# Optimization experiments

Hardware: AMD Instinct MI355X
Metric: run time of the kernel (lower is better)

## Reference

```python
import jax, jax.numpy as jnp
import numpy as np
from jax import lax

MAX_C = 16       # MAX_MERGE_NUMS
COND_THRES = 0.2
IOU_THRES = 0.3
CLASS_OFFSET = 1e4  # shift per-class so cross-class BEV IoU == 0 (emulates per-class loop)


def setup_inputs() -> dict:
    key = jax.random.key(0)
    k1, k2, k3, k4, k5 = jax.random.split(key, 5)
    B, N = 4, 4096
    # realistic 3D boxes: centers, positive sizes, heading
    centers = jax.random.normal(k1, (B, N, 3), jnp.float32) * 20.0
    sizes = jax.random.uniform(k2, (B, N, 3), jnp.float32, 0.5, 4.5)
    heading = jax.random.uniform(k3, (B, N, 1), jnp.float32, -np.pi, np.pi)
    boxes = jnp.concatenate([centers, sizes, heading], -1)  # [B,N,7]
    scores = jax.random.uniform(k4, (B, N), jnp.float32)
    labels = jax.random.randint(k5, (B, N), 0, 3, jnp.int32)
    kw = jax.random.split(jax.random.fold_in(key, 1), 2)
    W1 = jax.random.normal(kw[0], (7, 64), jnp.float32) * 0.3
    b1 = jnp.zeros((64,), jnp.float32)
    W2 = jax.random.normal(kw[1], (64, 1), jnp.float32) * 0.3
    b2 = jnp.zeros((1,), jnp.float32)
    return {"boxes": boxes, "scores": scores, "labels": labels,
            "W1": W1, "b1": b1, "W2": W2, "b2": b2}


def _nms_merge_frame(boxes, scores, labels, W1, b1, W2, b2):
    # boxes [N,7], scores [N], labels [N] int32
    N = boxes.shape[0]
    valid = scores > COND_THRES                       # cond_mask
    skey = jnp.where(valid, scores, -jnp.inf)
    order = jnp.argsort(-skey)                        # score descending
    boxes, scores = boxes[order], scores[order]
    labels, valid = labels[order], valid[order]

    # nearest-BEV (axis-aligned) IoU; class offset keeps classes disjoint
    off = labels.astype(boxes.dtype) * CLASS_OFFSET
    cx, cy = boxes[:, 0] + off, boxes[:, 1]
    hx, hy = boxes[:, 3] * 0.5, boxes[:, 4] * 0.5
    x1, x2, y1, y2 = cx - hx, cx + hx, cy - hy, cy + hy
    ix = jnp.clip(jnp.minimum(x2[:, None], x2[None]) - jnp.maximum(x1[:, None], x1[None]), 0.0)
    iy = jnp.clip(jnp.minimum(y2[:, None], y2[None]) - jnp.maximum(y1[:, None], y1[None]), 0.0)
    inter = ix * iy                                   # [N,N]
    area = (x2 - x1) * (y2 - y1)
    iou = inter / jnp.clip(area[:, None] + area[None] - inter, 1e-6)
    overlap = iou > IOU_THRES                         # includes self

    # greedy clustering: highest-score remaining box leads its cluster
    def body(i, st):
        alive, cid = st
        lead = alive[i]
        take = alive & overlap[i] & lead
        cid = jnp.where(take, i, cid)
        return alive & (~take), cid
    alive, cid = lax.fori_loop(0, N, body,
                               (valid, jnp.full((N,), -1, jnp.int32)))
    leader = cid == jnp.arange(N, dtype=jnp.int32)    # cluster representatives

    # rank of each box within its cluster (score order preserved)
    idx = jnp.arange(N)
    same = (cid[None, :] == cid[:, None]) & (cid[:, None] >= 0)
    rank = (same & (idx[None, :] < idx[:, None])).sum(-1)  # [N]

    # scatter up to MAX_C members per cluster (zero-padded buffers)
    dest = jnp.where((cid >= 0) & (rank < MAX_C), cid, N)  # N = dump row
    clusters = jnp.zeros((N + 1, MAX_C, 7), boxes.dtype)
    clusters = clusters.at[dest, jnp.minimum(rank, MAX_C - 1)].set(boxes)[:N]

    # merge network: per-box MLP -> softmax weights over cluster slots
    h = jax.nn.relu(clusters @ W1 + b1)               # [N,MAX_C,64]
    logits = (h @ W2 + b2)[..., 0]                    # [N,MAX_C]
    slot_ok = jnp.any(clusters != 0, -1)
    logits = jnp.where(slot_ok, logits, -1e9)
    w = jax.nn.softmax(logits, -1)
    merged = jnp.einsum('nc,ncd->nd', w, clusters)    # [N,7]

    # masked scatter: non-positive merged sizes fall back to leader sizes
    size = jnp.where(merged[:, 3:6] <= 0, boxes[:, 3:6], merged[:, 3:6])
    out_box = jnp.concatenate([merged[:, :3], size, merged[:, 6:7]], -1)
    info = jnp.concatenate([out_box, scores[:, None],
                            labels.astype(boxes.dtype)[:, None]], -1)  # [N,9]
    info = jnp.where(leader[:, None], info, 0.0)
    return info, leader


def reference(boxes, scores, labels, W1, b1, W2, b2):
    info, leader = jax.vmap(_nms_merge_frame,
                            in_axes=(0, 0, 0, None, None, None, None))(
        boxes, scores, labels, W1, b1, W2, b2)
    return info, leader
```

## Files before the change

kernel.cpp:

```cpp
#include <hip/hip_runtime.h>
#include <stdint.h>

#pragma clang fp contract(off)

#define BF 4
#define NN 4096
#define MAXC 16
#define PL 2048
#define WL 32
#define WF 24
#define TRI_CAP (64 * (WL * (WL + 1) / 2))

typedef unsigned long long u64;
typedef uint32_t u32;

#define WAVE_SYNC() asm volatile("s_waitcnt lgkmcnt(0)" ::: "memory")

__device__ __forceinline__ u64 shfl64(u64 v, int src) {
  return (u64)__shfl((long long)v, src, 64);
}
__device__ __forceinline__ u64 readlane64(u64 v, int l) {
  u32 lo = (u32)__builtin_amdgcn_readlane((int)(u32)v, l);
  u32 hi = (u32)__builtin_amdgcn_readlane((int)(u32)(v >> 32), l);
  return ((u64)hi << 32) | lo;
}
__device__ __forceinline__ u64 greedy64_iso(u64 D, u64 rem, u64 onlyme) {
  u64 lead = 0;
  while (rem) {
    u64 t = D & rem;
    u64 iso = __ballot(t == onlyme) & rem;
    lead |= iso;
    rem &= ~iso;
    if (!rem) break;
    int b = __builtin_ctzll(rem);
    lead |= 1ull << b;
    rem &= ~readlane64(D, b);
    if (!rem) break;
    b = __builtin_ctzll(rem);
    lead |= 1ull << b;
    rem &= ~readlane64(D, b);
  }
  return lead;
}

__global__ __launch_bounds__(256) void rank_kernel(
    const float* __restrict__ scores, u64* __restrict__ keyS)
{
  __shared__ u64 keys[NN];
  __shared__ int cnt[4][64];
  const int f = blockIdx.x >> 6, rb = blockIdx.x & 63;
  const int tid = threadIdx.x, wave = tid >> 6, lane = tid & 63;
  for (int s = 0; s < 16; s++) {
    int idx = tid + 256 * s;
    float sc = scores[f * NN + idx];
    bool valid = sc > 0.2f;
    u32 bits = __float_as_uint(sc);
    u32 m = bits ^ ((bits >> 31) ? 0xFFFFFFFFu : 0x80000000u);
    u32 hi = valid ? ~m : 0xFFFFFFFFu;
    keys[idx] = ((u64)hi << 32) | (u32)idx;
  }
  __syncthreads();
  const int row = rb * 64 + lane;
  const u64 mykey = keys[row];
  int c = 0;
  const int j0 = wave * 1024;
#pragma unroll 8
  for (int j = j0; j < j0 + 1024; j++)
    c += (keys[j] < mykey) ? 1 : 0;
  cnt[wave][lane] = c;
  __syncthreads();
  if (wave == 0) {
    int rank = cnt[0][lane] + cnt[1][lane] + cnt[2][lane] + cnt[3][lane];
    keyS[f * NN + rank] = mykey;
  }
}

__global__ __launch_bounds__(256) void countscan_kernel(
    const u64* __restrict__ keyS, const int* __restrict__ labels,
    int* __restrict__ chunkOffG, int* __restrict__ VbufL)
{
  __shared__ int cnt[64][3];
  const int f = blockIdx.x, tid = threadIdx.x;
  const int wave = tid >> 6, lane = tid & 63;
  for (int s = 0; s < 16; s++) {
    int chunk = wave * 16 + s;
    int p = chunk * 64 + lane;
    u64 kv = keyS[f * NN + p];
    bool valid = (u32)(kv >> 32) != 0xFFFFFFFFu;
    int g = (int)(kv & 0xFFFFFFFFull);
    int l = valid ? labels[f * NN + g] : 3;
    u64 B0 = __ballot((l & 1) != 0);
    u64 B1 = __ballot((l & 2) != 0);
    if (lane < 3) {
      u64 Mb = ((lane & 1) ? B0 : ~B0) & ((lane & 2) ? B1 : ~B1);
      cnt[chunk][lane] = __popcll(Mb);
    }
  }
  __syncthreads();
  if (wave == 0) {
    for (int ll = 0; ll < 3; ll++) {
      int v = cnt[lane][ll];
      int incl = v;
      for (int off2 = 1; off2 < 64; off2 <<= 1) {
        int up = __shfl_up(incl, off2, 64);
        if (lane >= off2) incl += up;
      }
      chunkOffG[(f * 64 + lane) * 3 + ll] = incl - v;
      if (lane == 63) VbufL[f * 3 + ll] = incl;
    }
  }
}

__global__ __launch_bounds__(256) void gather_kernel(
    const u64* __restrict__ keyS, const float* __restrict__ boxes,
    const float* __restrict__ scores, const int* __restrict__ labels,
    const int* __restrict__ chunkOffG,
    float* __restrict__ sboxes, float* __restrict__ sscore, float* __restrict__ slabel,
    int* __restrict__ lab_slot, int* __restrict__ loc_slot,
    int* __restrict__ pglob,
    float* __restrict__ px1, float* __restrict__ px2, float* __restrict__ py1,
    float* __restrict__ py2, float* __restrict__ parea)
{
  const int gs = blockIdx.x * 256 + threadIdx.x;
  const int f = gs >> 12, p = gs & (NN - 1);
  const int lane = threadIdx.x & 63, chunk = p >> 6;
  const u64 ltmask = (1ull << lane) - 1ull;
  u64 kv = keyS[gs];
  bool valid = (u32)(kv >> 32) != 0xFFFFFFFFu;
  int g = (int)(kv & 0xFFFFFFFFull);
  const float* bp = boxes + (size_t)(f * NN + g) * 7;
  float b0 = bp[0], b1v = bp[1], b2v = bp[2], b3 = bp[3], b4 = bp[4], b5 = bp[5], b6 = bp[6];
  int lab = labels[f * NN + g];
  const int o = f * NN + p;
  float* sb = sboxes + (size_t)o * 7;
  sb[0] = b0; sb[1] = b1v; sb[2] = b2v; sb[3] = b3; sb[4] = b4; sb[5] = b5; sb[6] = b6;
  sscore[o] = scores[f * NN + g];
  slabel[o] = (float)lab;
  int l = valid ? lab : 3;
  u64 B0 = __ballot((l & 1) != 0);
  u64 B1 = __ballot((l & 2) != 0);
  u64 M = ((l & 1) ? B0 : ~B0) & ((l & 2) ? B1 : ~B1);
  int rank = __popcll(M & ltmask);
  if (l < 3) {
    int loc = chunkOffG[(f * 64 + chunk) * 3 + l] + rank;
    int pi = (f * 3 + l) * PL + loc;
    float off = (float)l * 10000.0f;
    float cx = b0 + off, cy = b1v;
    float hx = b3 * 0.5f, hy = b4 * 0.5f;
    float x1 = cx - hx, x2 = cx + hx, y1 = cy - hy, y2 = cy + hy;
    float area = (x2 - x1) * (y2 - y1);
    pglob[pi] = p;
    px1[pi] = x1; px2[pi] = x2; py1[pi] = y1; py2[pi] = y2; parea[pi] = area;
    lab_slot[o] = l; loc_slot[o] = loc;
  } else {
    lab_slot[o] = -1; loc_slot[o] = -1;
  }
}

__global__ __launch_bounds__(256) void mask_kernel(
    const float* __restrict__ px1, const float* __restrict__ px2,
    const float* __restrict__ py1, const float* __restrict__ py2,
    const float* __restrict__ parea, const int* __restrict__ pglob,
    const int* __restrict__ VbufL,
    u64* __restrict__ maskP, u64* __restrict__ triT)
{
  __shared__ float4 cbox[1024];
  __shared__ float carea[1024];
  const int bx = blockIdx.x;
  const int fl = bx >> 8, rem = bx & 255;
  const int rt = rem >> 1, wt = rem & 1;
  const int r0 = rt * 16;
  const int Vl = VbufL[fl];
  if (r0 >= Vl) return;
  if (wt * 1024 >= Vl) return;
  const int tid = threadIdx.x;
  for (int q = tid; q < 1024; q += 256) {
    int c = fl * PL + wt * 1024 + q;
    cbox[q] = make_float4(px1[c], px2[c], py1[c], py2[c]);
    carea[q] = parea[c];
  }
  __syncthreads();
  const int row = r0 + (tid & 15);
  const int wl = tid >> 4;
  const int cw = wt * 16 + wl;
  const int nc = Vl - cw * 64;
  if (row >= Vl || nc <= 0) return;
  const int rg = fl * PL + row;
  const float rx1 = px1[rg], rx2 = px2[rg], ry1 = py1[rg], ry2 = py2[rg], ra = parea[rg];
  u64 bits = 0;
  const int qb = wl * 64;
  for (int b = 0; b < 64; b++) {
    float4 cb = cbox[qb + b];
    float ca = carea[qb + b];
    float ix = fminf(rx2, cb.y) - fmaxf(rx1, cb.x);
    ix = fmaxf(ix, 0.0f);
    float iy = fminf(ry2, cb.w) - fmaxf(ry1, cb.z);
    iy = fmaxf(iy, 0.0f);
    float inter = ix * iy;
    float den = fmaxf((ra + ca) - inter, 1e-6f);
    float iou = inter / den;
    bits |= ((u64)(iou > 0.3f)) << b;
  }
  if (nc < 64) bits &= (1ull << nc) - 1ull;
  const int f = fl / 3;
  const int p = pglob[fl * PL + row];
  maskP[((size_t)f * NN + p) * WL + cw] = bits;
  if (row >= 64 * cw) {
    const int W = (Vl + 63) >> 6;
    int base = 64 * (cw * W - (cw * (cw - 1)) / 2);
    triT[(size_t)fl * TRI_CAP + base + (row - 64 * cw)] = bits;
  }
}

__global__ __launch_bounds__(64) void nms_kernel(
    const u64* __restrict__ triT, const int* __restrict__ VbufL,
    u64* __restrict__ leadersP)
{
  __shared__ u64 tri[64 * (WF * (WF + 1) / 2) + 128];
  const int fl = blockIdx.x, lane = threadIdx.x;
  const int Vl = VbufL[fl];
  const int W = (Vl + 63) >> 6;
  const u64* mT = triT + (size_t)fl * TRI_CAP;
  const u64 onlyme = 1ull << lane;
  u64 alive = 0;
  if (lane < WL) {
    int rb = Vl - 64 * lane;
    alive = (rb >= 64) ? ~0ull : ((rb > 0) ? ((1ull << rb) - 1ull) : 0ull);
  }
  u64 myLead = 0;

  if (W > 0 && W <= WF) {
    const int totw = 64 * (W * (W + 1) / 2);
    const int nch = (totw * 8 + 1023) >> 10;
    const char* g = (const char*)mT;
    char* l = (char*)tri;
    int batch = 0;
    for (int it = 0; it < nch; it++) {
      __builtin_amdgcn_global_load_lds(
          (const __attribute__((address_space(1))) unsigned int*)(g + (size_t)it * 1024 + (size_t)lane * 16),
          (__attribute__((address_space(3))) unsigned int*)(l + (size_t)it * 1024),
          16, 0, 0);
      if (++batch == 48) {
        asm volatile("s_waitcnt vmcnt(0)" ::: "memory");
        batch = 0;
      }
    }
    asm volatile("s_waitcnt vmcnt(0)" ::: "memory");
    int offw = 0;
    u64 D = tri[lane];
    for (int w = 0; w < W; w++) {
      const int offw_next = offw + 64 * (W - w);
      u64 Dnext = (w + 1 < W) ? tri[offw_next + lane] : 0;
      u64 lead = greedy64_iso(D, readlane64(alive, w), onlyme);
      if (lane == w) myLead = lead;
      if (lead) {
        const u64* strm = tri + offw;
        int v = w + 1;
        for (; v + 3 < W; v += 4) {
          u64 a0 = strm[64 * (v - w) + lane];
          u64 a1 = strm[64 * (v + 1 - w) + lane];
          u64 a2 = strm[64 * (v + 2 - w) + lane];
          u64 a3 = strm[64 * (v + 3 - w) + lane];
          u64 c0 = __ballot((a0 & lead) != 0ull);
          u64 c1 = __ballot((a1 & lead) != 0ull);
          u64 c2 = __ballot((a2 & lead) != 0ull);
          u64 c3 = __ballot((a3 & lead) != 0ull);
          if (lane == v)     alive &= ~c0;
          if (lane == v + 1) alive &= ~c1;
          if (lane == v + 2) alive &= ~c2;
          if (lane == v + 3) alive &= ~c3;
        }
        for (; v < W; v++) {
          u64 a0 = strm[64 * (v - w) + lane];
          u64 c0 = __ballot((a0 & lead) != 0ull);
          if (lane == v) alive &= ~c0;
        }
      }
      D = Dnext;
      offw = offw_next;
    }
  } else if (W > 0) {
    int offw = 0;
    for (int w = 0; w < W; w++) {
      const u64* strm = mT + offw;
      u64 D = strm[lane];
      u64 lead = greedy64_iso(D, readlane64(alive, w), onlyme);
      if (lane == w) myLead = lead;
      if (lead) {
        for (int v = w + 1; v < W; v++) {
          u64 a0 = strm[64 * (v - w) + lane];
          u64 c0 = __ballot((a0 & lead) != 0ull);
          if (lane == v) alive &= ~c0;
        }
      }
      offw += 64 * (W - w);
    }
  }
  if (lane < WL) leadersP[fl * WL + lane] = myLead;
}

__global__ __launch_bounds__(256) void cid_kernel(
    const u64* __restrict__ maskP, const u64* __restrict__ leadersP,
    const int* __restrict__ lab_slot, const int* __restrict__ loc_slot,
    const int* __restrict__ VbufL, int* __restrict__ cidP)
{
  const int g = blockIdx.x * 4 + (threadIdx.x >> 6);
  const int lane = threadIdx.x & 63;
  const int f = g >> 12, p = g & (NN - 1);
  const int l = lab_slot[f * NN + p];
  if (l < 0) return;
  const int fl = f * 3 + l;
  const int loc = loc_slot[f * NN + p];
  const int Wl = (VbufL[fl] + 63) >> 6;
  u64 L = 0, m = 0;
  if (lane < Wl) {
    L = leadersP[fl * WL + lane];
    m = maskP[((size_t)f * NN + p) * WL + lane];
  }
  const int g6 = loc >> 6, b6 = loc & 63;
  u64 pmask = (lane < g6) ? ~0ull
            : (lane == g6 ? ((b6 == 63) ? ~0ull : ((1ull << (b6 + 1)) - 1ull)) : 0ull);
  u64 v = m & L & pmask;
  u64 bl = __ballot(v != 0ull);
  int cid = -1;
  if (bl != 0ull) {
    int w = __builtin_ctzll(bl);
    u64 vw = shfl64(v, w);
    cid = w * 64 + __builtin_ctzll(vw);
  }
  if (lane == 0) cidP[fl * PL + loc] = cid;
}

__global__ __launch_bounds__(256) void mm_kernel(
    const u64* __restrict__ maskP, const u64* __restrict__ leadersP,
    const int* __restrict__ cidP, const int* __restrict__ lab_slot,
    const int* __restrict__ loc_slot, const int* __restrict__ pglob,
    const int* __restrict__ VbufL,
    const float* __restrict__ sboxes, const float* __restrict__ sscore,
    const float* __restrict__ slabel,
    const float* __restrict__ W1, const float* __restrict__ b1,
    const float* __restrict__ W2, const float* __restrict__ b2,
    float* __restrict__ out)
{
  __shared__ int   mlistS[4][MAXC];
  __shared__ float mbS[4][MAXC][7];
  __shared__ float lgS[4][MAXC];
  __shared__ float wnS[4][MAXC];
  const int wv = threadIdx.x >> 6, lane = threadIdx.x & 63;
  const int bi = blockIdx.x * 4 + wv;
  const int f = bi >> 12, i = bi & (NN - 1);
  const int o = f * NN + i;
  float* info = out + (size_t)o * 9;
  float* lead = out + (size_t)BF * NN * 9 + o;
  const int l = lab_slot[o];
  bool isLead = false;
  int loc = 0, fl = 0;
  if (l >= 0) {
    fl = f * 3 + l;
    loc = loc_slot[o];
    isLead = (leadersP[fl * WL + (loc >> 6)] >> (loc & 63)) & 1ull;
  }
  if (!isLead) {
    if (lane < 9) info[lane] = 0.0f;
    if (lane == 0) *lead = 0.0f;
    return;
  }
  int* mlist = mlistS[wv];
  float (*mb)[7] = mbS[wv];
  float* lg = lgS[wv];
  float* wn = wnS[wv];
  const u64* mrow = maskP + (size_t)o * WL;
  const int Wl = (VbufL[fl] + 63) >> 6;
  int total = 0;
  for (int w = loc >> 6; w < Wl && total < MAXC; w++) {
    u64 word = mrow[w];
    int pos = w * 64 + lane;
    bool cand = ((word >> lane) & 1ull) && (cidP[fl * PL + pos] == loc);
    u64 mbal = __ballot(cand);
    int r = __popcll(mbal & ((1ull << lane) - 1ull));
    int slot = total + r;
    if (cand && slot < MAXC) mlist[slot] = pglob[fl * PL + pos];
    total += __popcll(mbal);
  }
  const int cnt = min(total, MAXC);
  WAVE_SYNC();
  if (lane < cnt) {
    int j = mlist[lane];
    const float* bp = sboxes + (size_t)(f * NN + j) * 7;
    for (int d = 0; d < 7; d++) mb[lane][d] = bp[d];
  }
  float w1r[7];
  for (int d = 0; d < 7; d++) w1r[d] = W1[d * 64 + lane];
  const float b1c = b1[lane], w2c = W2[lane], b2v = b2[0];
  WAVE_SYNC();
  for (int s = 0; s < cnt; s++) {
    float t = b1c;
    for (int d = 0; d < 7; d++) t += mb[s][d] * w1r[d];
    float h = fmaxf(t, 0.0f);
    float v = h * w2c;
    for (int off2 = 32; off2 > 0; off2 >>= 1) v += __shfl_xor(v, off2, 64);
    if (lane == 0) lg[s] = v + b2v;
  }
  WAVE_SYNC();
  float mx = -1e30f;
  for (int s = 0; s < cnt; s++) mx = fmaxf(mx, lg[s]);
  float den = 0.0f;
  for (int s = 0; s < cnt; s++) den += expf(lg[s] - mx);
  if (lane < cnt) wn[lane] = expf(lg[lane] - mx) / den;
  WAVE_SYNC();
  float val = 0.0f;
  if (lane < 7) {
    float acc = 0.0f;
    for (int s = 0; s < cnt; s++) acc += wn[s] * mb[s][lane];
    val = acc;
    if (lane >= 3 && lane <= 5 && val <= 0.0f) val = sboxes[(size_t)o * 7 + lane];
  } else if (lane == 7) {
    val = sscore[o];
  } else if (lane == 8) {
    val = slabel[o];
  }
  if (lane < 9) info[lane] = val;
  if (lane == 0) *lead = 1.0f;
}

extern "C" void kernel_launch(void* const* d_in, const int* in_sizes, int n_in,
                              void* d_out, int out_size, void* d_ws, size_t ws_size,
                              hipStream_t stream)
{
  const float* boxes  = (const float*)d_in[0];
  const float* scores = (const float*)d_in[1];
  const int*   labels = (const int*)d_in[2];
  const float* W1     = (const float*)d_in[3];
  const float* b1     = (const float*)d_in[4];
  const float* W2     = (const float*)d_in[5];
  const float* b2     = (const float*)d_in[6];
  float* out = (float*)d_out;

  char* ws = (char*)d_ws;
  size_t off = 0;
  auto alloc = [&](size_t bytes) -> void* {
    void* p = ws + off;
    off = (off + bytes + 255) & ~(size_t)255;
    return p;
  };
  u64*   keyS    = (u64*)  alloc((size_t)BF * NN * 8);
  int*   chunkOffG=(int*)  alloc((size_t)BF * 64 * 3 * 4);
  float* sboxes  = (float*)alloc((size_t)BF * NN * 7 * 4);
  float* sscore  = (float*)alloc((size_t)BF * NN * 4);
  float* slabel  = (float*)alloc((size_t)BF * NN * 4);
  int*   lab_slot= (int*)  alloc((size_t)BF * NN * 4);
  int*   loc_slot= (int*)  alloc((size_t)BF * NN * 4);
  int*   pglob   = (int*)  alloc((size_t)BF * 3 * PL * 4);
  float* px1     = (float*)alloc((size_t)BF * 3 * PL * 4);
  float* px2     = (float*)alloc((size_t)BF * 3 * PL * 4);
  float* py1     = (float*)alloc((size_t)BF * 3 * PL * 4);
  float* py2     = (float*)alloc((size_t)BF * 3 * PL * 4);
  float* parea   = (float*)alloc((size_t)BF * 3 * PL * 4);
  int*   VbufL   = (int*)  alloc((size_t)BF * 3 * 4);
  u64*   leadersP= (u64*)  alloc((size_t)BF * 3 * WL * 8);
  int*   cidP    = (int*)  alloc((size_t)BF * 3 * PL * 4);
  u64*   maskP   = (u64*)  alloc((size_t)BF * NN * WL * 8);
  u64*   triT    = (u64*)  alloc((size_t)BF * 3 * TRI_CAP * 8);
  (void)  alloc(32768);

  rank_kernel<<<BF * 64, 256, 0, stream>>>(scores, keyS);
  countscan_kernel<<<BF, 256, 0, stream>>>(keyS, labels, chunkOffG, VbufL);
  gather_kernel<<<BF * NN / 256, 256, 0, stream>>>(keyS, boxes, scores, labels,
                                                   chunkOffG, sboxes, sscore,
                                                   slabel, lab_slot, loc_slot,
                                                   pglob, px1, px2, py1, py2,
                                                   parea);
  mask_kernel<<<BF * 3 * 256, 256, 0, stream>>>(px1, px2, py1, py2, parea,
                                                pglob, VbufL, maskP, triT);
  nms_kernel<<<BF * 3, 64, 0, stream>>>(triT, VbufL, leadersP);
  cid_kernel<<<BF * NN / 4, 256, 0, stream>>>(maskP, leadersP, lab_slot,
                                              loc_slot, VbufL, cidP);
  mm_kernel<<<BF * NN / 4, 256, 0, stream>>>(maskP, leadersP, cidP, lab_slot,
                                             loc_slot, pglob, VbufL, sboxes,
                                             sscore, slabel, W1, b1, W2, b2, out);
}
```

Baseline: 159.6 us.

## Fuse rank, per-label count/scan and gather into one kernel

Label bits are packed into the low bits of each sort key. The rank kernel now counts, for each element, both its global rank and its rank within its own label, and scatters the boxes and per-class arrays directly. This removes the countscan and gather kernels, the keyS and chunkOffG intermediates, and two launches. Each thread does slightly more work in the O(N) comparison loop. Separately, the mask kernel now loads only the valid columns into shared memory.

After: 156.8 us. Within noise of the previous version (-1.8%).

```diff
diff --git a/kernel.cpp b/kernel.cpp
--- a/kernel.cpp
+++ b/kernel.cpp
@@ -43,117 +43,91 @@
   return lead;
 }
 
-__global__ __launch_bounds__(256) void rank_kernel(
-    const float* __restrict__ scores, u64* __restrict__ keyS)
+__global__ __launch_bounds__(256) void rg_kernel(
+    const float* __restrict__ scores, const float* __restrict__ boxes,
+    const int* __restrict__ labels,
+    float* __restrict__ sboxes, float* __restrict__ sscore, float* __restrict__ slabel,
+    int* __restrict__ lab_slot, int* __restrict__ loc_slot,
+    int* __restrict__ pglob,
+    float* __restrict__ px1, float* __restrict__ px2, float* __restrict__ py1,
+    float* __restrict__ py2, float* __restrict__ parea,
+    int* __restrict__ VbufL)
 {
   __shared__ u64 keys[NN];
   __shared__ int cnt[4][64];
+  __shared__ int lcnt[4][64];
+  __shared__ int vc[4][3];
   const int f = blockIdx.x >> 6, rb = blockIdx.x & 63;
   const int tid = threadIdx.x, wave = tid >> 6, lane = tid & 63;
   for (int s = 0; s < 16; s++) {
     int idx = tid + 256 * s;
     float sc = scores[f * NN + idx];
     bool valid = sc > 0.2f;
+    int lab = labels[f * NN + idx];
     u32 bits = __float_as_uint(sc);
     u32 m = bits ^ ((bits >> 31) ? 0xFFFFFFFFu : 0x80000000u);
     u32 hi = valid ? ~m : 0xFFFFFFFFu;
-    keys[idx] = ((u64)hi << 32) | (u32)idx;
+    u32 lo = ((u32)idx << 2) | (valid ? (u32)lab : 3u);
+    keys[idx] = ((u64)hi << 32) | lo;
   }
   __syncthreads();
+  if (rb == 0) {
+    int c0 = 0, c1 = 0, c2 = 0;
+    const int base = wave * 1024;
+    for (int s = 0; s < 16; s++) {
+      u32 lb = (u32)keys[base + s * 64 + lane] & 3u;
+      c0 += (lb == 0); c1 += (lb == 1); c2 += (lb == 2);
+    }
+    for (int off = 32; off; off >>= 1) {
+      c0 += __shfl_xor(c0, off, 64);
+      c1 += __shfl_xor(c1, off, 64);
+      c2 += __shfl_xor(c2, off, 64);
+    }
+    if (lane == 0) { vc[wave][0] = c0; vc[wave][1] = c1; vc[wave][2] = c2; }
+  }
   const int row = rb * 64 + lane;
   const u64 mykey = keys[row];
-  int c = 0;
+  const u32 mylab = (u32)mykey & 3u;
+  int c = 0, lc = 0;
   const int j0 = wave * 1024;
 #pragma unroll 8
-  for (int j = j0; j < j0 + 1024; j++)
-    c += (keys[j] < mykey) ? 1 : 0;
+  for (int j = j0; j < j0 + 1024; j++) {
+    u64 kj = keys[j];
+    bool lt = kj < mykey;
+    c += lt ? 1 : 0;
+    lc += (lt && (((u32)kj & 3u) == mylab)) ? 1 : 0;
+  }
   cnt[wave][lane] = c;
+  lcnt[wave][lane] = lc;
   __syncthreads();
+  if (rb == 0 && wave == 1 && lane < 3)
+    VbufL[f * 3 + lane] = vc[0][lane] + vc[1][lane] + vc[2][lane] + vc[3][lane];
   if (wave == 0) {
     int rank = cnt[0][lane] + cnt[1][lane] + cnt[2][lane] + cnt[3][lane];
-    keyS[f * NN + rank] = mykey;
-  }
-}
-
-__global__ __launch_bounds__(256) void countscan_kernel(
-    const u64* __restrict__ keyS, const int* __restrict__ labels,
-    int* __restrict__ chunkOffG, int* __restrict__ VbufL)
-{
-  __shared__ int cnt[64][3];
-  const int f = blockIdx.x, tid = threadIdx.x;
-  const int wave = tid >> 6, lane = tid & 63;
-  for (int s = 0; s < 16; s++) {
-    int chunk = wave * 16 + s;
-    int p = chunk * 64 + lane;
-    u64 kv = keyS[f * NN + p];
-    bool valid = (u32)(kv >> 32) != 0xFFFFFFFFu;
-    int g = (int)(kv & 0xFFFFFFFFull);
-    int l = valid ? labels[f * NN + g] : 3;
-    u64 B0 = __ballot((l & 1) != 0);
-    u64 B1 = __ballot((l & 2) != 0);
-    if (lane < 3) {
-      u64 Mb = ((lane & 1) ? B0 : ~B0) & ((lane & 2) ? B1 : ~B1);
-      cnt[chunk][lane] = __popcll(Mb);
-    }
-  }
-  __syncthreads();
-  if (wave == 0) {
-    for (int ll = 0; ll < 3; ll++) {
-      int v = cnt[lane][ll];
-      int incl = v;
-      for (int off2 = 1; off2 < 64; off2 <<= 1) {
-        int up = __shfl_up(incl, off2, 64);
-        if (lane >= off2) incl += up;
-      }
-      chunkOffG[(f * 64 + lane) * 3 + ll] = incl - v;
-      if (lane == 63) VbufL[f * 3 + ll] = incl;
-    }
-  }
-}
-
-__global__ __launch_bounds__(256) void gather_kernel(
-    const u64* __restrict__ keyS, const float* __restrict__ boxes,
-    const float* __restrict__ scores, const int* __restrict__ labels,
-    const int* __restrict__ chunkOffG,
-    float* __restrict__ sboxes, float* __restrict__ sscore, float* __restrict__ slabel,
-    int* __restrict__ lab_slot, int* __restrict__ loc_slot,
-    int* __restrict__ pglob,
-    float* __restrict__ px1, float* __restrict__ px2, float* __restrict__ py1,
-    float* __restrict__ py2, float* __restrict__ parea)
-{
-  const int gs = blockIdx.x * 256 + threadIdx.x;
-  const int f = gs >> 12, p = gs & (NN - 1);
-  const int lane = threadIdx.x & 63, chunk = p >> 6;
-  const u64 ltmask = (1ull << lane) - 1ull;
-  u64 kv = keyS[gs];
-  bool valid = (u32)(kv >> 32) != 0xFFFFFFFFu;
-  int g = (int)(kv & 0xFFFFFFFFull);
-  const float* bp = boxes + (size_t)(f * NN + g) * 7;
-  float b0 = bp[0], b1v = bp[1], b2v = bp[2], b3 = bp[3], b4 = bp[4], b5 = bp[5], b6 = bp[6];
-  int lab = labels[f * NN + g];
-  const int o = f * NN + p;
-  float* sb = sboxes + (size_t)o * 7;
-  sb[0] = b0; sb[1] = b1v; sb[2] = b2v; sb[3] = b3; sb[4] = b4; sb[5] = b5; sb[6] = b6;
-  sscore[o] = scores[f * NN + g];
-  slabel[o] = (float)lab;
-  int l = valid ? lab : 3;
-  u64 B0 = __ballot((l & 1) != 0);
-  u64 B1 = __ballot((l & 2) != 0);
-  u64 M = ((l & 1) ? B0 : ~B0) & ((l & 2) ? B1 : ~B1);
-  int rank = __popcll(M & ltmask);
-  if (l < 3) {
-    int loc = chunkOffG[(f * 64 + chunk) * 3 + l] + rank;
-    int pi = (f * 3 + l) * PL + loc;
-    float off = (float)l * 10000.0f;
-    float cx = b0 + off, cy = b1v;
-    float hx = b3 * 0.5f, hy = b4 * 0.5f;
-    float x1 = cx - hx, x2 = cx + hx, y1 = cy - hy, y2 = cy + hy;
-    float area = (x2 - x1) * (y2 - y1);
-    pglob[pi] = p;
-    px1[pi] = x1; px2[pi] = x2; py1[pi] = y1; py2[pi] = y2; parea[pi] = area;
-    lab_slot[o] = l; loc_slot[o] = loc;
-  } else {
-    lab_slot[o] = -1; loc_slot[o] = -1;
+    int loc  = lcnt[0][lane] + lcnt[1][lane] + lcnt[2][lane] + lcnt[3][lane];
+    const int i = row;
+    const float* bp = boxes + (size_t)(f * NN + i) * 7;
+    float b0 = bp[0], b1v = bp[1], b2v = bp[2], b3 = bp[3], b4 = bp[4], b5 = bp[5], b6 = bp[6];
+    int lab = labels[f * NN + i];
+    float sc = scores[f * NN + i];
+    const int o = f * NN + rank;
+    float* sb = sboxes + (size_t)o * 7;
+    sb[0] = b0; sb[1] = b1v; sb[2] = b2v; sb[3] = b3; sb[4] = b4; sb[5] = b5; sb[6] = b6;
+    sscore[o] = sc;
+    slabel[o] = (float)lab;
+    if (mylab < 3u) {
+      int pi = (f * 3 + (int)mylab) * PL + loc;
+      float off = (float)mylab * 10000.0f;
+      float cx = b0 + off, cy = b1v;
+      float hx = b3 * 0.5f, hy = b4 * 0.5f;
+      float x1 = cx - hx, x2 = cx + hx, y1 = cy - hy, y2 = cy + hy;
+      float area = (x2 - x1) * (y2 - y1);
+      pglob[pi] = rank;
+      px1[pi] = x1; px2[pi] = x2; py1[pi] = y1; py2[pi] = y2; parea[pi] = area;
+      lab_slot[o] = (int)mylab; loc_slot[o] = loc;
+    } else {
+      lab_slot[o] = -1; loc_slot[o] = -1;
+    }
   }
 }
 
@@ -174,7 +148,9 @@
   if (r0 >= Vl) return;
   if (wt * 1024 >= Vl) return;
   const int tid = threadIdx.x;
-  for (int q = tid; q < 1024; q += 256) {
+  const int ncol = Vl - wt * 1024;
+  const int nload = (ncol < 1024) ? ncol : 1024;
+  for (int q = tid; q < nload; q += 256) {
     int c = fl * PL + wt * 1024 + q;
     cbox[q] = make_float4(px1[c], px2[c], py1[c], py2[c]);
     carea[q] = parea[c];
@@ -443,8 +419,6 @@
     off = (off + bytes + 255) & ~(size_t)255;
     return p;
   };
-  u64*   keyS    = (u64*)  alloc((size_t)BF * NN * 8);
-  int*   chunkOffG=(int*)  alloc((size_t)BF * 64 * 3 * 4);
   float* sboxes  = (float*)alloc((size_t)BF * NN * 7 * 4);
   float* sscore  = (float*)alloc((size_t)BF * NN * 4);
   float* slabel  = (float*)alloc((size_t)BF * NN * 4);
@@ -463,13 +437,10 @@
   u64*   triT    = (u64*)  alloc((size_t)BF * 3 * TRI_CAP * 8);
   (void)  alloc(32768);
 
-  rank_kernel<<<BF * 64, 256, 0, stream>>>(scores, keyS);
-  countscan_kernel<<<BF, 256, 0, stream>>>(keyS, labels, chunkOffG, VbufL);
-  gather_kernel<<<BF * NN / 256, 256, 0, stream>>>(keyS, boxes, scores, labels,
-                                                   chunkOffG, sboxes, sscore,
-                                                   slabel, lab_slot, loc_slot,
-                                                   pglob, px1, px2, py1, py2,
-                                                   parea);
+  rg_kernel<<<BF * 64, 256, 0, stream>>>(scores, boxes, labels, sboxes,
+                                         sscore, slabel, lab_slot, loc_slot,
+                                         pglob, px1, px2, py1, py2, parea,
+                                         VbufL);
   mask_kernel<<<BF * 3 * 256, 256, 0, stream>>>(px1, px2, py1, py2, parea,
                                                 pglob, VbufL, maskP, triT);
   nms_kernel<<<BF * 3, 64, 0, stream>>>(triT, VbufL, leadersP);
```
